# Kernel optimization log

Hardware: AMD Instinct MI355X
Metric: run time of the kernel (lower is better)

Reference implementation:

```python
import jax, jax.numpy as jnp
import numpy as np

N_FEAT = 64      # number of continuous features
N_BINS = 255     # bin edges per feature (EBM default) -> 256 score slots incl. OOV
N_PAIRS = 32     # interaction terms
BATCH = 262144


def _bin_indices(edges, x):
    """TF Discretization (searchsorted right) + IntegerLookup(vocab=range(B), OOV->0).
    edges: [N, B] sorted per row; x: [batch, N] -> int32 [batch, N] in [0, B]."""
    idx = jax.vmap(lambda e, col: jnp.searchsorted(e, col, side='right'),
                   in_axes=(0, 1), out_axes=1)(edges, x)  # [batch, N], values 0..B
    B = edges.shape[1]
    # IntegerLookup: value v in {0..B-1} -> v+1 ; value B (not in vocab) -> OOV index 0
    return jnp.where(idx < B, idx + 1, 0)


def setup_inputs() -> dict:
    key = jax.random.key(0)
    ks = jax.random.split(key, 6)
    x = jax.random.normal(ks[0], (BATCH, N_FEAT), dtype=jnp.float32)
    edges = jnp.sort(jax.random.normal(ks[1], (N_FEAT, N_BINS), dtype=jnp.float32), axis=1)
    pair_edges = jnp.sort(jax.random.normal(ks[2], (N_FEAT, N_BINS), dtype=jnp.float32), axis=1)
    w = jax.random.normal(ks[3], (N_FEAT, N_BINS + 1), dtype=jnp.float32) * 0.1
    tables = jax.random.normal(ks[4], (N_PAIRS, N_BINS + 1, N_BINS + 1), dtype=jnp.float32) * 0.1
    pairs = jax.random.randint(ks[5], (N_PAIRS, 2), 0, N_FEAT, dtype=jnp.int32)
    bias = jnp.zeros((1,), dtype=jnp.float32)
    return {"x": x, "edges": edges, "w": w, "pair_edges": pair_edges,
            "pairs": pairs, "tables": tables, "bias": bias}


def reference(x, edges, w, pair_edges, pairs, tables, bias):
    # --- per-feature main effects: one_hot(idx) @ Dense(1) == gather w[f, idx] ---
    idx = _bin_indices(edges, x)                                  # [batch, N]
    feat = w[jnp.arange(N_FEAT)[None, :], idx]                    # [batch, N]
    # --- pairwise interactions: gather_nd on [L, R] lookup tables ---
    pidx = _bin_indices(pair_edges, x)                            # [batch, N]
    li = pidx[:, pairs[:, 0]]                                     # [batch, P]
    ri = pidx[:, pairs[:, 1]]                                     # [batch, P]
    inter = tables[jnp.arange(N_PAIRS)[None, :], li, ri]          # [batch, P]
    # --- BiasLayer: reduce_sum(concat, axis=1) + bias, then sigmoid ---
    logits = jnp.sum(feat, axis=1) + jnp.sum(inter, axis=1) + bias[0]
    return jax.nn.sigmoid(logits)                                  # [batch]
```

## Files before the change

### kernel.cpp

```cpp
#include <hip/hip_runtime.h>
#include <hip/hip_fp16.h>

#define NBINS 255
#define NPAIRS 32
#define BIGF 3.0e38f


__global__ void ebm_prep(const float* __restrict__ edges,
                         const float* __restrict__ pair_edges,
                         const float* __restrict__ w,
                         float* __restrict__ ws) {
    int tid = blockIdx.x * blockDim.x + threadIdx.x;
    int f = tid >> 8, j = tid & 255;
    float* E  = ws;
    float* PE = ws + 16384;
    float* ME = ws + 32768;
    float* MP = ws + 36864;
    float* CU = ws + 40960;
    float* CP = ws + 41984;
    __half* W = (__half*)(ws + 43008);
    E[tid]  = (j < NBINS) ? edges[f * NBINS + j]      : BIGF;
    PE[tid] = (j < NBINS) ? pair_edges[f * NBINS + j] : BIGF;
    int src = (j < 255) ? j + 1 : 0;
    W[tid]  = __float2half(w[f * 256 + src]);
    if (j < 64) {
        int idx = 4 * j + 3;
        ME[f * 64 + j] = (idx < NBINS) ? edges[f * NBINS + idx]      : BIGF;
        MP[f * 64 + j] = (idx < NBINS) ? pair_edges[f * NBINS + idx] : BIGF;
    }
    if (j < 16) {
        CU[f * 16 + j] = (j < 15) ? edges[f * NBINS + 16 * j + 15]      : BIGF;
        CP[f * 16 + j] = (j < 15) ? pair_edges[f * NBINS + 16 * j + 15] : BIGF;
    }
}

__global__ void ebm_prep_tables(const float* __restrict__ tables,
                                unsigned short* __restrict__ o) {
    int i = blockIdx.x * blockDim.x + threadIdx.x;
    int b = i & 255, a = (i >> 8) & 255, p = i >> 16;
    int ra = (a < 255) ? a + 1 : 0;
    int rb = (b < 255) ? b + 1 : 0;
    o[i] = __half_as_ushort(__float2half(tables[(p << 16) + (ra << 8) + rb]));
}

__device__ __forceinline__ unsigned pick16(const unsigned* pw, int s) {
    unsigned v01 = (s & 1) ? pw[1]  : pw[0];
    unsigned v23 = (s & 1) ? pw[3]  : pw[2];
    unsigned v45 = (s & 1) ? pw[5]  : pw[4];
    unsigned v67 = (s & 1) ? pw[7]  : pw[6];
    unsigned v89 = (s & 1) ? pw[9]  : pw[8];
    unsigned vab = (s & 1) ? pw[11] : pw[10];
    unsigned vcd = (s & 1) ? pw[13] : pw[12];
    unsigned vef = (s & 1) ? pw[15] : pw[14];
    unsigned w0 = (s & 2) ? v23 : v01;
    unsigned w1 = (s & 2) ? v67 : v45;
    unsigned w2 = (s & 2) ? vab : v89;
    unsigned w3 = (s & 2) ? vef : vcd;
    unsigned u0 = (s & 4) ? w1 : w0;
    unsigned u1 = (s & 4) ? w3 : w2;
    return (s & 8) ? u1 : u0;
}

__global__ __launch_bounds__(1024, 4) void ebm_main(
    const float* __restrict__ x,
    const int*   __restrict__ pairs,
    const float* __restrict__ tables_f32,
    const float* __restrict__ bias,
    const float* __restrict__ ws,
    const __half* __restrict__ T16,
    int useT16,
    float*       __restrict__ out) {

    __shared__ float  sE[16384];
    __shared__ float  sPE[16384];
    __shared__ float4 sME[1024];
    __shared__ float4 sMP[1024];

    int tid = threadIdx.x;
    {
        const float4* w4 = (const float4*)ws;
        float4* dE = (float4*)sE;
        float4* dP = (float4*)sPE;
        for (int i = tid; i < 4096; i += 1024) {
            dE[i] = w4[i];
            dP[i] = w4[4096 + i];
        }
        sME[tid] = w4[8192 + tid];
        sMP[tid] = w4[9216 + tid];
    }
    const float*  CU = ws + 40960;
    const float*  CP = ws + 41984;
    const __half* Wg = (const __half*)(ws + 43008);
    float bias0 = bias[0];

    __syncthreads();

    int row = blockIdx.x * 1024 + tid;
    const float4* x4  = (const float4*)x + row * 16;
    const float4* sE4 = (const float4*)sE;
    const float4* sP4 = (const float4*)sPE;

    float acc = 0.f;
    unsigned pw[16];

    float4 xa = x4[0];
    float4 xb = x4[1];
#pragma unroll
    for (int gg = 0; gg < 8; ++gg) {
        int fb = gg * 8;
        float4 xan = xa, xbn = xb;
        if (gg < 7) { xan = x4[2 * gg + 2]; xbn = x4[2 * gg + 3]; }
        float xf[8] = {xa.x, xa.y, xa.z, xa.w, xb.x, xb.y, xb.z, xb.w};

        int t[8], t2[8];
#pragma unroll
        for (int j = 0; j < 8; ++j) {
            const float* cu = CU + (fb + j) * 16;
            int tt = 0;
#pragma unroll
            for (int k = 0; k < 15; ++k) tt += (xf[j] >= cu[k]);
            t[j] = tt;
        }
#pragma unroll
        for (int j = 0; j < 8; ++j) {
            const float* cp = CP + (fb + j) * 16;
            int tt = 0;
#pragma unroll
            for (int k = 0; k < 15; ++k) tt += (xf[j] >= cp[k]);
            t2[j] = tt;
        }
        float4 mu[8], mp[8];
#pragma unroll
        for (int j = 0; j < 8; ++j) mu[j] = sME[(fb + j) * 16 + t[j]];
#pragma unroll
        for (int j = 0; j < 8; ++j) mp[j] = sMP[(fb + j) * 16 + t2[j]];
        int lo[8], lo2[8];
        float4 fu[8], fp[8];
#pragma unroll
        for (int j = 0; j < 8; ++j) {
            int m = (xf[j] >= mu[j].x) + (xf[j] >= mu[j].y) + (xf[j] >= mu[j].z);
            lo[j] = 4 * t[j] + m;
            fu[j] = sE4[(fb + j) * 64 + lo[j]];
        }
#pragma unroll
        for (int j = 0; j < 8; ++j) {
            int m = (xf[j] >= mp[j].x) + (xf[j] >= mp[j].y) + (xf[j] >= mp[j].z);
            lo2[j] = 4 * t2[j] + m;
            fp[j] = sP4[(fb + j) * 64 + lo2[j]];
        }
#pragma unroll
        for (int j = 0; j < 8; ++j) {
            int c = 4 * lo[j] + (xf[j] >= fu[j].x) + (xf[j] >= fu[j].y) +
                    (xf[j] >= fu[j].z) + (xf[j] >= fu[j].w);
            acc += __half2float(Wg[(fb + j) * 256 + c]);
        }
        unsigned p0 = 0, p1 = 0;
#pragma unroll
        for (int j = 0; j < 4; ++j) {
            int c2 = 4 * lo2[j] + (xf[j] >= fp[j].x) + (xf[j] >= fp[j].y) +
                     (xf[j] >= fp[j].z) + (xf[j] >= fp[j].w);
            p0 |= (unsigned)c2 << (8 * j);
        }
#pragma unroll
        for (int j = 4; j < 8; ++j) {
            int c2 = 4 * lo2[j] + (xf[j] >= fp[j].x) + (xf[j] >= fp[j].y) +
                     (xf[j] >= fp[j].z) + (xf[j] >= fp[j].w);
            p1 |= (unsigned)c2 << (8 * (j - 4));
        }
        pw[2 * gg]     = p0;
        pw[2 * gg + 1] = p1;
        xa = xan; xb = xbn;
    }

    if (useT16) {
#pragma unroll
        for (int p = 0; p < NPAIRS; ++p) {
            int a = pairs[2 * p], b = pairs[2 * p + 1];
            unsigned wa = pick16(pw, a >> 2);
            unsigned wb = pick16(pw, b >> 2);
            int li = (wa >> ((a & 3) * 8)) & 255;
            int ri = (wb >> ((b & 3) * 8)) & 255;
            acc += __half2float(T16[(p << 16) + (li << 8) + ri]);
        }
    } else {
#pragma unroll
        for (int p = 0; p < NPAIRS; ++p) {
            int a = pairs[2 * p], b = pairs[2 * p + 1];
            unsigned wa = pick16(pw, a >> 2);
            unsigned wb = pick16(pw, b >> 2);
            int li = (wa >> ((a & 3) * 8)) & 255;
            int ri = (wb >> ((b & 3) * 8)) & 255;
            int lb = (li < 255) ? li + 1 : 0;
            int rb = (ri < 255) ? ri + 1 : 0;
            acc += tables_f32[(p << 16) + (lb << 8) + rb];
        }
    }

    out[row] = 1.0f / (1.0f + __expf(-(acc + bias0)));
}

extern "C" void kernel_launch(void* const* d_in, const int* in_sizes, int n_in,
                              void* d_out, int out_size, void* d_ws, size_t ws_size,
                              hipStream_t stream) {
    const float* x          = (const float*)d_in[0];
    const float* edges      = (const float*)d_in[1];
    const float* w          = (const float*)d_in[2];
    const float* pair_edges = (const float*)d_in[3];
    const int*   pairs      = (const int*)d_in[4];
    const float* tables     = (const float*)d_in[5];
    const float* bias       = (const float*)d_in[6];
    float* out = (float*)d_out;
    float* ws  = (float*)d_ws;

    int useT16 = (ws_size >= (size_t)4399104) ? 1 : 0;
    __half* T16 = (__half*)((char*)d_ws + 204800);

    ebm_prep<<<64, 256, 0, stream>>>(edges, pair_edges, w, ws);
    if (useT16) {
        ebm_prep_tables<<<2048, 1024, 0, stream>>>(tables, (unsigned short*)T16);
    }
    ebm_main<<<256, 1024, 0, stream>>>(x, pairs, tables, bias, ws, T16, useT16, out);
}
```

Before: 192.3 us.

## Replace hierarchical bin search with sigmoid-mapped guess table plus short linear probe

Maps each input through a sigmoid-like transform onto 256 cells and stores, per feature and cell, a starting group index for both edge sets in a shared-memory guess table. The main kernel then checks one or two float4 groups and walks forward only as far as needed, replacing the two-level compare cascade over coarse and mid edge arrays. This cuts comparison and LDS traffic per feature, but brings in data-dependent while loops that can diverge, and it relies on the Gaussian-shaped edge distribution so the initial guesses land close to the right group.

```diff
diff --git a/kernel.cpp b/kernel.cpp
--- a/kernel.cpp
+++ b/kernel.cpp
@@ -5,33 +5,40 @@
 #define NPAIRS 32
 #define BIGF 3.0e38f
 
+
+__device__ __forceinline__ int cell_of(float x) {
+    float h = __builtin_amdgcn_exp2f(-2.4567f * x);
+    float u = __builtin_amdgcn_rcpf(1.0f + h);
+    int c = (int)(u * 256.0f);
+    c = c < 0 ? 0 : c;
+    c = c > 255 ? 255 : c;
+    return c;
+}
 
 __global__ void ebm_prep(const float* __restrict__ edges,
                          const float* __restrict__ pair_edges,
                          const float* __restrict__ w,
                          float* __restrict__ ws) {
-    int tid = blockIdx.x * blockDim.x + threadIdx.x;
-    int f = tid >> 8, j = tid & 255;
+    int f = blockIdx.x, j = threadIdx.x;
     float* E  = ws;
     float* PE = ws + 16384;
-    float* ME = ws + 32768;
-    float* MP = ws + 36864;
-    float* CU = ws + 40960;
-    float* CP = ws + 41984;
+    unsigned short* G = (unsigned short*)(ws + 32768);
     __half* W = (__half*)(ws + 43008);
-    E[tid]  = (j < NBINS) ? edges[f * NBINS + j]      : BIGF;
-    PE[tid] = (j < NBINS) ? pair_edges[f * NBINS + j] : BIGF;
+    E[f * 256 + j]  = (j < NBINS) ? edges[f * NBINS + j]      : BIGF;
+    PE[f * 256 + j] = (j < NBINS) ? pair_edges[f * NBINS + j] : BIGF;
     int src = (j < 255) ? j + 1 : 0;
-    W[tid]  = __float2half(w[f * 256 + src]);
-    if (j < 64) {
-        int idx = 4 * j + 3;
-        ME[f * 64 + j] = (idx < NBINS) ? edges[f * NBINS + idx]      : BIGF;
-        MP[f * 64 + j] = (idx < NBINS) ? pair_edges[f * NBINS + idx] : BIGF;
-    }
-    if (j < 16) {
-        CU[f * 16 + j] = (j < 15) ? edges[f * NBINS + 16 * j + 15]      : BIGF;
-        CP[f * 16 + j] = (j < 15) ? pair_edges[f * NBINS + 16 * j + 15] : BIGF;
-    }
+    W[f * 256 + j]  = __float2half(w[f * 256 + src]);
+
+    __shared__ int bu[63], bp[63];
+    if (j < 63) {
+        bu[j] = cell_of(edges[f * NBINS + 4 * j + 3]);
+        bp[j] = cell_of(pair_edges[f * NBINS + 4 * j + 3]);
+    }
+    __syncthreads();
+    int gu = 0, gp = 0;
+#pragma unroll
+    for (int g = 0; g < 63; ++g) { gu += (bu[g] < j); gp += (bp[g] < j); }
+    G[f * 256 + j] = (unsigned short)(gu | (gp << 8));
 }
 
 __global__ void ebm_prep_tables(const float* __restrict__ tables,
@@ -73,23 +80,20 @@
 
     __shared__ float  sE[16384];
     __shared__ float  sPE[16384];
-    __shared__ float4 sME[1024];
-    __shared__ float4 sMP[1024];
+    __shared__ unsigned short sG[16384];
 
     int tid = threadIdx.x;
     {
         const float4* w4 = (const float4*)ws;
         float4* dE = (float4*)sE;
         float4* dP = (float4*)sPE;
+        float4* dG = (float4*)sG;
         for (int i = tid; i < 4096; i += 1024) {
             dE[i] = w4[i];
             dP[i] = w4[4096 + i];
         }
-        sME[tid] = w4[8192 + tid];
-        sMP[tid] = w4[9216 + tid];
-    }
-    const float*  CU = ws + 40960;
-    const float*  CP = ws + 41984;
+        for (int i = tid; i < 2048; i += 1024) dG[i] = w4[8192 + i];
+    }
     const __half* Wg = (const __half*)(ws + 43008);
     float bias0 = bias[0];
 
@@ -112,60 +116,39 @@
         if (gg < 7) { xan = x4[2 * gg + 2]; xbn = x4[2 * gg + 3]; }
         float xf[8] = {xa.x, xa.y, xa.z, xa.w, xb.x, xb.y, xb.z, xb.w};
 
-        int t[8], t2[8];
+        unsigned gw[8];
 #pragma unroll
         for (int j = 0; j < 8; ++j) {
-            const float* cu = CU + (fb + j) * 16;
-            int tt = 0;
-#pragma unroll
-            for (int k = 0; k < 15; ++k) tt += (xf[j] >= cu[k]);
-            t[j] = tt;
-        }
+            int cell = cell_of(xf[j]);
+            gw[j] = sG[(fb + j) * 256 + cell];
+        }
+
+        unsigned p0 = 0, p1 = 0;
 #pragma unroll
         for (int j = 0; j < 8; ++j) {
-            const float* cp = CP + (fb + j) * 16;
-            int tt = 0;
-#pragma unroll
-            for (int k = 0; k < 15; ++k) tt += (xf[j] >= cp[k]);
-            t2[j] = tt;
-        }
-        float4 mu[8], mp[8];
-#pragma unroll
-        for (int j = 0; j < 8; ++j) mu[j] = sME[(fb + j) * 16 + t[j]];
-#pragma unroll
-        for (int j = 0; j < 8; ++j) mp[j] = sMP[(fb + j) * 16 + t2[j]];
-        int lo[8], lo2[8];
-        float4 fu[8], fp[8];
-#pragma unroll
-        for (int j = 0; j < 8; ++j) {
-            int m = (xf[j] >= mu[j].x) + (xf[j] >= mu[j].y) + (xf[j] >= mu[j].z);
-            lo[j] = 4 * t[j] + m;
-            fu[j] = sE4[(fb + j) * 64 + lo[j]];
-        }
-#pragma unroll
-        for (int j = 0; j < 8; ++j) {
-            int m = (xf[j] >= mp[j].x) + (xf[j] >= mp[j].y) + (xf[j] >= mp[j].z);
-            lo2[j] = 4 * t2[j] + m;
-            fp[j] = sP4[(fb + j) * 64 + lo2[j]];
-        }
-#pragma unroll
-        for (int j = 0; j < 8; ++j) {
-            int c = 4 * lo[j] + (xf[j] >= fu[j].x) + (xf[j] >= fu[j].y) +
-                    (xf[j] >= fu[j].z) + (xf[j] >= fu[j].w);
+            float xv = xf[j];
+            int g0u = gw[j] & 255;
+            int g0p = gw[j] >> 8;
+            int ebase = (fb + j) * 64;
+
+            float4 a0 = sE4[ebase + g0u];
+            float4 a1 = sE4[ebase + g0u + 1];
+            bool du = xv >= a0.w;
+            int gu2 = g0u + du;
+            float4 fa = du ? a1 : a0;
+            while (xv >= fa.w) { ++gu2; fa = sE4[ebase + gu2]; }
+            int c = 4 * gu2 + (xv >= fa.x) + (xv >= fa.y) + (xv >= fa.z);
             acc += __half2float(Wg[(fb + j) * 256 + c]);
-        }
-        unsigned p0 = 0, p1 = 0;
-#pragma unroll
-        for (int j = 0; j < 4; ++j) {
-            int c2 = 4 * lo2[j] + (xf[j] >= fp[j].x) + (xf[j] >= fp[j].y) +
-                     (xf[j] >= fp[j].z) + (xf[j] >= fp[j].w);
-            p0 |= (unsigned)c2 << (8 * j);
-        }
-#pragma unroll
-        for (int j = 4; j < 8; ++j) {
-            int c2 = 4 * lo2[j] + (xf[j] >= fp[j].x) + (xf[j] >= fp[j].y) +
-                     (xf[j] >= fp[j].z) + (xf[j] >= fp[j].w);
-            p1 |= (unsigned)c2 << (8 * (j - 4));
+
+            float4 b0 = sP4[ebase + g0p];
+            float4 b1 = sP4[ebase + g0p + 1];
+            bool dp = xv >= b0.w;
+            int gp2 = g0p + dp;
+            float4 fpv = dp ? b1 : b0;
+            while (xv >= fpv.w) { ++gp2; fpv = sP4[ebase + gp2]; }
+            int c2 = 4 * gp2 + (xv >= fpv.x) + (xv >= fpv.y) + (xv >= fpv.z);
+            if (j < 4) p0 |= (unsigned)c2 << (8 * j);
+            else       p1 |= (unsigned)c2 << (8 * (j - 4));
         }
         pw[2 * gg]     = p0;
         pw[2 * gg + 1] = p1;
```

Result: slower. 312.4 us (+62.4%).
